# Optimization experiments

Measured on AMD Instinct MI355X. Metric: run time of the kernel, lower is better.

The kernel has to match this reference:

```python
import jax, jax.numpy as jnp
import numpy as np

GRID_SIZE = 20
GRID_MIN, GRID_MAX = -2.0, 2.0
SIGMA = (GRID_MAX - GRID_MIN) / (GRID_SIZE - 1)  # RBF width = grid spacing


def setup_inputs() -> dict:
    key = jax.random.key(0)
    k1, k2, k3 = jax.random.split(key, 3)
    batch, in_features, out_features = 4096, 1024, 1024
    x = jax.random.normal(k1, (batch, in_features), dtype=jnp.float32)
    # glorot-scale initializations for faithfulness to keras glorot_uniform magnitude
    lim_b = np.sqrt(6.0 / (in_features + out_features))
    base_weight = jax.random.uniform(k2, (in_features, out_features), jnp.float32, -lim_b, lim_b)
    lim_s = np.sqrt(6.0 / (in_features * GRID_SIZE + out_features))
    spline_weight = jax.random.uniform(k3, (in_features, GRID_SIZE, out_features), jnp.float32, -lim_s, lim_s)
    mu = jnp.linspace(GRID_MIN, GRID_MAX, GRID_SIZE, dtype=jnp.float32)
    return {"x": x, "base_weight": base_weight, "spline_weight": spline_weight, "mu": mu}


def reference(x, base_weight, spline_weight, mu):
    # base path: SiLU(x) @ W_base
    base_out = jnp.einsum('bi,io->bo', jax.nn.silu(x), base_weight)
    # RBF basis expansion: [b, i, g]
    diff = (x[..., None] - mu) / SIGMA
    basis = jnp.exp(-(diff * diff))
    spline_out = jnp.einsum('big,igo->bo', basis, spline_weight)
    return base_out + spline_out
```

## Files before the change

kernel.cpp:

```cpp
#include <hip/hip_runtime.h>
#include <hip/hip_bf16.h>
#include <stdint.h>


typedef short short8 __attribute__((ext_vector_type(8)));
typedef __bf16 bf16x8 __attribute__((ext_vector_type(8)));
typedef float f32x4 __attribute__((ext_vector_type(4)));
typedef unsigned int u32;

__device__ __forceinline__ unsigned short f2bf(float f) {
  __hip_bfloat16 h = __float2bfloat16(f);
  return __builtin_bit_cast(unsigned short, h);
}

__device__ __forceinline__ void gload_lds16(const unsigned short* g, unsigned short* l) {
  __builtin_amdgcn_global_load_lds(
      (const __attribute__((address_space(1))) u32*)(const void*)g,
      (__attribute__((address_space(3))) u32*)(void*)l, 16, 0, 0);
}


__global__ void prep_silu(const float* __restrict__ x, unsigned short* __restrict__ A1) {
  int g = blockIdx.x * 256 + threadIdx.x;
  const float4* x4 = reinterpret_cast<const float4*>(x);
  float4 a = x4[g * 2], b = x4[g * 2 + 1];
  float v[8] = {a.x, a.y, a.z, a.w, b.x, b.y, b.z, b.w};
  union { unsigned short u[8]; short8 v8; } o;
#pragma unroll
  for (int j = 0; j < 8; ++j) {
    float s = v[j] / (1.f + __expf(-v[j]));
    o.u[j] = f2bf(s);
  }
  *reinterpret_cast<short8*>(&A1[(size_t)g * 8]) = o.v8;
}

__global__ void prep_basis(const float* __restrict__ x, unsigned short* __restrict__ A2,
                           int i0, int L) {
  int g = blockIdx.x * 256 + threadIdx.x;
  int e0 = g * 8;
  int b = e0 / L;
  int k0 = e0 - b * L;
  const float* xr = x + (size_t)b * 1024 + i0;
  union { unsigned short u[8]; short8 v8; } o;
#pragma unroll
  for (int j = 0; j < 8; ++j) {
    int k = k0 + j;
    int il = (int)(((unsigned)k * 104858u) >> 21);
    int gg = k - il * 20;
    float xv = xr[il];
    float d = (xv + 2.0f) * 4.75f - (float)gg;
    o.u[j] = f2bf(__expf(-d * d));
  }
  *reinterpret_cast<short8*>(&A2[(size_t)b * L + k0]) = o.v8;
}

__global__ void prep_wt(const float* __restrict__ W, unsigned short* __restrict__ Bt, int Kp) {
  __shared__ unsigned short tile[64][72];
  int tiles_k = Kp >> 6;
  int bk = blockIdx.x % tiles_k, bn = blockIdx.x / tiles_k;
  int t = threadIdx.x;
  int lr = t >> 4;
  int lc = (t & 15) * 4;
#pragma unroll
  for (int r = 0; r < 4; ++r) {
    int row = r * 16 + lr;
    float4 v = *reinterpret_cast<const float4*>(&W[(size_t)(bk * 64 + row) * 1024 + bn * 64 + lc]);
    tile[row][lc + 0] = f2bf(v.x);
    tile[row][lc + 1] = f2bf(v.y);
    tile[row][lc + 2] = f2bf(v.z);
    tile[row][lc + 3] = f2bf(v.w);
  }
  __syncthreads();
  int nr = t >> 3;
  int kc = (t & 7) * 8;
#pragma unroll
  for (int r = 0; r < 2; ++r) {
    int n = r * 32 + nr;
    union { unsigned short u[8]; short8 v8; } o;
#pragma unroll
    for (int j = 0; j < 8; ++j) o.u[j] = tile[kc + j][n];
    *reinterpret_cast<short8*>(&Bt[(size_t)(bn * 64 + n) * Kp + bk * 64 + kc]) = o.v8;
  }
}

template <bool ATOMIC>
__global__ __launch_bounds__(256, 4) void gemm_bf16(
    const unsigned short* __restrict__ A, int lda,
    const unsigned short* __restrict__ Bt, int ldb,
    float* __restrict__ C, int Kz) {
  const int tid = threadIdx.x;
  const int wid = tid >> 6, lane = tid & 63;

  const int cpx = gridDim.x >> 3;
  const int wg = (blockIdx.x & 7) * cpx + (blockIdx.x >> 3);
  const int mtile = wg & 31;
  const int ntile = (wg >> 5) & 7;
  const int z = wg >> 8;
  const int brow = mtile * 128, bcol = ntile * 128;
  const int kbase = z * Kz;

  __shared__ __align__(16) unsigned short As[128 * 64];
  __shared__ __align__(16) unsigned short Bs[128 * 64];

  const int srow = wid * 32 + (lane >> 3);
  const int scol = (lane & 7) * 8;
  const unsigned short* aptr = A + (size_t)(brow + srow) * lda + kbase + scol;
  const unsigned short* bptr = Bt + (size_t)(bcol + srow) * ldb + kbase + scol;
  unsigned short* lA = &As[wid * 2048];
  unsigned short* lB = &Bs[wid * 2048];

  const int wr = wid >> 1, wc = wid & 1;
  const int fr = lane & 15;
  const int fk = (lane >> 4) * 8;

  f32x4 acc[4][4] = {};

  for (int kt = 0; kt < Kz; kt += 64) {
#pragma unroll
    for (int c = 0; c < 4; ++c)
      gload_lds16(aptr + (size_t)(c * 8) * lda, lA + c * 512);
#pragma unroll
    for (int c = 0; c < 4; ++c)
      gload_lds16(bptr + (size_t)(c * 8) * ldb, lB + c * 512);
    aptr += 64;
    bptr += 64;
    __syncthreads();
#pragma unroll
    for (int ks = 0; ks < 2; ++ks) {
      bf16x8 af[4], bfr[4];
#pragma unroll
      for (int m = 0; m < 4; ++m)
        af[m] = __builtin_bit_cast(
            bf16x8, *reinterpret_cast<const short8*>(
                        &As[(wr * 64 + m * 16 + fr) * 64 + ks * 32 + fk]));
#pragma unroll
      for (int n = 0; n < 4; ++n)
        bfr[n] = __builtin_bit_cast(
            bf16x8, *reinterpret_cast<const short8*>(
                        &Bs[(wc * 64 + n * 16 + fr) * 64 + ks * 32 + fk]));
#pragma unroll
      for (int m = 0; m < 4; ++m)
#pragma unroll
        for (int n = 0; n < 4; ++n)
          acc[m][n] = __builtin_amdgcn_mfma_f32_16x16x32_bf16(af[m], bfr[n], acc[m][n], 0, 0, 0);
    }
    __syncthreads();
  }

  const int r0 = brow + wr * 64 + (lane >> 4) * 4;
  const int c0 = bcol + wc * 64 + (lane & 15);
#pragma unroll
  for (int m = 0; m < 4; ++m)
#pragma unroll
    for (int n = 0; n < 4; ++n)
#pragma unroll
      for (int j = 0; j < 4; ++j) {
        size_t idx = (size_t)(r0 + m * 16 + j) * 1024 + (c0 + n * 16);
        float v = acc[m][n][j];
        if (ATOMIC)
          atomicAdd(&C[idx], v);
        else
          C[idx] = v;
      }
}


extern "C" void kernel_launch(void* const* d_in, const int* in_sizes, int n_in,
                              void* d_out, int out_size, void* d_ws, size_t ws_size,
                              hipStream_t stream) {
  (void)in_sizes; (void)n_in; (void)out_size;
  const float* x = (const float*)d_in[0];
  const float* Wb = (const float*)d_in[1];
  const float* Ws = (const float*)d_in[2];
  float* out = (float*)d_out;
  char* ws = (char*)d_ws;

  const size_t A1_off = 0;
  const size_t W1t_off = 8388608;
  const size_t dyn_off = W1t_off + 2097152;
  unsigned short* A1  = (unsigned short*)(ws + A1_off);
  unsigned short* W1t = (unsigned short*)(ws + W1t_off);

  int npass = 16;
  for (int np = 2; np <= 16; np <<= 1) {
    size_t CI = 1024 / np;
    size_t need = dyn_off + 4096ull * CI * 20 * 2 + CI * 20 * 1024 * 2;
    if (need <= ws_size) { npass = np; break; }
  }
  const int CI = 1024 / npass;
  const int Kp = CI * 20;
  const int Kz = Kp / 4;
  unsigned short* A2  = (unsigned short*)(ws + dyn_off);
  unsigned short* W2t = (unsigned short*)(ws + dyn_off + 4096ull * CI * 20 * 2);

  prep_silu<<<2048, 256, 0, stream>>>(x, A1);
  prep_wt<<<256, 256, 0, stream>>>(Wb, W1t, 1024);
  gemm_bf16<false><<<256, 256, 0, stream>>>(A1, 1024, W1t, 1024, out, 1024);

  for (int p = 0; p < npass; ++p) {
    const int nb_basis = 4096 * Kp / 8 / 256;
    prep_basis<<<nb_basis, 256, 0, stream>>>(x, A2, p * CI, Kp);
    prep_wt<<<(Kp / 64) * 16, 256, 0, stream>>>(Ws + (size_t)p * Kp * 1024, W2t, Kp);
    gemm_bf16<true><<<1024, 256, 0, stream>>>(A2, Kp, W2t, Kp, out, Kz);
  }
}
```

Measured before the change: 474.9 us.

## Swizzle LDS layout and fold base GEMM into first spline pass

Applies an XOR swizzle to the LDS tile layout for both the global-to-LDS load and the MFMA fragment reads, to reduce bank conflicts on 128-byte row strides. It also concatenates the SiLU activations and base weights with the first spline chunk along K, so the base projection runs inside the first split-K GEMM instead of a separate launch. The output is zeroed with a memset and all GEMM writes are now atomic adds. This removes one GEMM launch and its tail, but makes the first pass larger and every store atomic.

```diff
diff --git a/kernel.cpp b/kernel.cpp
--- a/kernel.cpp
+++ b/kernel.cpp
@@ -20,8 +20,10 @@
 }
 
 
-__global__ void prep_silu(const float* __restrict__ x, unsigned short* __restrict__ A1) {
+__global__ void prep_silu(const float* __restrict__ x, unsigned short* __restrict__ A, int ld) {
   int g = blockIdx.x * 256 + threadIdx.x;
+  int row = g >> 7;
+  int col = (g & 127) * 8;
   const float4* x4 = reinterpret_cast<const float4*>(x);
   float4 a = x4[g * 2], b = x4[g * 2 + 1];
   float v[8] = {a.x, a.y, a.z, a.w, b.x, b.y, b.z, b.w};
@@ -31,11 +33,11 @@
     float s = v[j] / (1.f + __expf(-v[j]));
     o.u[j] = f2bf(s);
   }
-  *reinterpret_cast<short8*>(&A1[(size_t)g * 8]) = o.v8;
-}
-
-__global__ void prep_basis(const float* __restrict__ x, unsigned short* __restrict__ A2,
-                           int i0, int L) {
+  *reinterpret_cast<short8*>(&A[(size_t)row * ld + col]) = o.v8;
+}
+
+__global__ void prep_basis(const float* __restrict__ x, unsigned short* __restrict__ A,
+                           int i0, int L, int ld, int col_off) {
   int g = blockIdx.x * 256 + threadIdx.x;
   int e0 = g * 8;
   int b = e0 / L;
@@ -51,10 +53,11 @@
     float d = (xv + 2.0f) * 4.75f - (float)gg;
     o.u[j] = f2bf(__expf(-d * d));
   }
-  *reinterpret_cast<short8*>(&A2[(size_t)b * L + k0]) = o.v8;
-}
-
-__global__ void prep_wt(const float* __restrict__ W, unsigned short* __restrict__ Bt, int Kp) {
+  *reinterpret_cast<short8*>(&A[(size_t)b * ld + col_off + k0]) = o.v8;
+}
+
+__global__ void prep_wt(const float* __restrict__ W, unsigned short* __restrict__ Bt,
+                        int Kp, int ldbt, int k_off) {
   __shared__ unsigned short tile[64][72];
   int tiles_k = Kp >> 6;
   int bk = blockIdx.x % tiles_k, bn = blockIdx.x / tiles_k;
@@ -79,11 +82,10 @@
     union { unsigned short u[8]; short8 v8; } o;
 #pragma unroll
     for (int j = 0; j < 8; ++j) o.u[j] = tile[kc + j][n];
-    *reinterpret_cast<short8*>(&Bt[(size_t)(bn * 64 + n) * Kp + bk * 64 + kc]) = o.v8;
-  }
-}
-
-template <bool ATOMIC>
+    *reinterpret_cast<short8*>(&Bt[(size_t)(bn * 64 + n) * ldbt + k_off + bk * 64 + kc]) = o.v8;
+  }
+}
+
 __global__ __launch_bounds__(256, 4) void gemm_bf16(
     const unsigned short* __restrict__ A, int lda,
     const unsigned short* __restrict__ Bt, int ldb,
@@ -103,7 +105,7 @@
   __shared__ __align__(16) unsigned short Bs[128 * 64];
 
   const int srow = wid * 32 + (lane >> 3);
-  const int scol = (lane & 7) * 8;
+  const int scol = ((lane & 7) ^ (lane >> 3)) * 8;
   const unsigned short* aptr = A + (size_t)(brow + srow) * lda + kbase + scol;
   const unsigned short* bptr = Bt + (size_t)(bcol + srow) * ldb + kbase + scol;
   unsigned short* lA = &As[wid * 2048];
@@ -111,7 +113,7 @@
 
   const int wr = wid >> 1, wc = wid & 1;
   const int fr = lane & 15;
-  const int fk = (lane >> 4) * 8;
+  const int fg = lane >> 4;
 
   f32x4 acc[4][4] = {};
 
@@ -129,15 +131,19 @@
     for (int ks = 0; ks < 2; ++ks) {
       bf16x8 af[4], bfr[4];
 #pragma unroll
-      for (int m = 0; m < 4; ++m)
+      for (int m = 0; m < 4; ++m) {
+        int row = wr * 64 + m * 16 + fr;
+        int cp = ((ks * 4 + fg) ^ (fr & 7)) * 8;
         af[m] = __builtin_bit_cast(
-            bf16x8, *reinterpret_cast<const short8*>(
-                        &As[(wr * 64 + m * 16 + fr) * 64 + ks * 32 + fk]));
-#pragma unroll
-      for (int n = 0; n < 4; ++n)
+            bf16x8, *reinterpret_cast<const short8*>(&As[row * 64 + cp]));
+      }
+#pragma unroll
+      for (int n = 0; n < 4; ++n) {
+        int row = wc * 64 + n * 16 + fr;
+        int cp = ((ks * 4 + fg) ^ (fr & 7)) * 8;
         bfr[n] = __builtin_bit_cast(
-            bf16x8, *reinterpret_cast<const short8*>(
-                        &Bs[(wc * 64 + n * 16 + fr) * 64 + ks * 32 + fk]));
+            bf16x8, *reinterpret_cast<const short8*>(&Bs[row * 64 + cp]));
+      }
 #pragma unroll
       for (int m = 0; m < 4; ++m)
 #pragma unroll
@@ -156,11 +162,7 @@
 #pragma unroll
       for (int j = 0; j < 4; ++j) {
         size_t idx = (size_t)(r0 + m * 16 + j) * 1024 + (c0 + n * 16);
-        float v = acc[m][n][j];
-        if (ATOMIC)
-          atomicAdd(&C[idx], v);
-        else
-          C[idx] = v;
+        atomicAdd(&C[idx], acc[m][n][j]);
       }
 }
 
@@ -175,32 +177,29 @@
   float* out = (float*)d_out;
   char* ws = (char*)d_ws;
 
-  const size_t A1_off = 0;
-  const size_t W1t_off = 8388608;
-  const size_t dyn_off = W1t_off + 2097152;
-  unsigned short* A1  = (unsigned short*)(ws + A1_off);
-  unsigned short* W1t = (unsigned short*)(ws + W1t_off);
-
   int npass = 16;
   for (int np = 2; np <= 16; np <<= 1) {
-    size_t CI = 1024 / np;
-    size_t need = dyn_off + 4096ull * CI * 20 * 2 + CI * 20 * 1024 * 2;
+    size_t K0 = 1024 + (1024 / np) * 20;
+    size_t need = 4096ull * K0 * 2 + 1024ull * K0 * 2;
     if (need <= ws_size) { npass = np; break; }
   }
   const int CI = 1024 / npass;
-  const int Kp = CI * 20;
-  const int Kz = Kp / 4;
-  unsigned short* A2  = (unsigned short*)(ws + dyn_off);
-  unsigned short* W2t = (unsigned short*)(ws + dyn_off + 4096ull * CI * 20 * 2);
-
-  prep_silu<<<2048, 256, 0, stream>>>(x, A1);
-  prep_wt<<<256, 256, 0, stream>>>(Wb, W1t, 1024);
-  gemm_bf16<false><<<256, 256, 0, stream>>>(A1, 1024, W1t, 1024, out, 1024);
+  const int K0 = 1024 + CI * 20;
+  const int Ksp = CI * 20;
+  unsigned short* A2  = (unsigned short*)ws;
+  unsigned short* W2t = (unsigned short*)(ws + 4096ull * K0 * 2);
+
+  hipMemsetAsync(out, 0, 4096ull * 1024 * 4, stream);
 
   for (int p = 0; p < npass; ++p) {
-    const int nb_basis = 4096 * Kp / 8 / 256;
-    prep_basis<<<nb_basis, 256, 0, stream>>>(x, A2, p * CI, Kp);
-    prep_wt<<<(Kp / 64) * 16, 256, 0, stream>>>(Ws + (size_t)p * Kp * 1024, W2t, Kp);
-    gemm_bf16<true><<<1024, 256, 0, stream>>>(A2, Kp, W2t, Kp, out, Kz);
-  }
-}
+    const int Kfull = (p == 0) ? K0 : Ksp;
+    const int col_off = (p == 0) ? 1024 : 0;
+    if (p == 0) {
+      prep_silu<<<2048, 256, 0, stream>>>(x, A2, Kfull);
+      prep_wt<<<256, 256, 0, stream>>>(Wb, W2t, 1024, Kfull, 0);
+    }
+    prep_basis<<<4096 * Ksp / 8 / 256, 256, 0, stream>>>(x, A2, p * CI, Ksp, Kfull, col_off);
+    prep_wt<<<(Ksp / 64) * 16, 256, 0, stream>>>(Ws + (size_t)p * Ksp * 1024, W2t, Ksp, Kfull, col_off);
+    gemm_bf16<<<1024, 256, 0, stream>>>(A2, Kfull, W2t, Kfull, out, Kfull / 4);
+  }
+}
```

After: 436.8 us. 8.0% less time.
